# Kernel optimization log

Hardware: AMD Instinct MI355X
Metric: run time of the kernel (lower is better)

Reference implementation:

```python
import jax, jax.numpy as jnp
import numpy as np

N_KERNELS = 11

def _kernel_mus(n):
    l = [1.0]
    bs = 2.0 / (n - 1)
    l.append(1 - bs / 2)
    for i in range(1, n - 1):
        l.append(l[i] - bs)
    return l

def _kernel_sigmas(n):
    bs = 2.0 / (n - 1)
    return [0.001] + [0.5 * bs] * (n - 1)

MU = jnp.asarray(_kernel_mus(N_KERNELS), jnp.float32)      # [K]
SIGMA = jnp.asarray(_kernel_sigmas(N_KERNELS), jnp.float32)  # [K]


def setup_inputs() -> dict:
    key = jax.random.key(0)
    ks = jax.random.split(key, 10)
    V, E, C = 50000, 300, 128
    B, Q, D = 128, 30, 200
    inp = {
        'query_tokens': jax.random.randint(ks[0], (B, Q), 0, V),
        'document_tokens': jax.random.randint(ks[1], (B, D), 0, V),
        'embedding': jax.random.normal(ks[2], (V, E), jnp.float32) * 0.1,
        'conv_w1': jax.random.normal(ks[3], (C, E, 1), jnp.float32) * 0.05,
        'conv_w2': jax.random.normal(ks[4], (C, E, 2), jnp.float32) * 0.05,
        'conv_w3': jax.random.normal(ks[5], (C, E, 3), jnp.float32) * 0.05,
        'conv_b1': jax.random.normal(ks[6], (C,), jnp.float32) * 0.01,
        'conv_b2': jax.random.normal(ks[7], (C,), jnp.float32) * 0.01,
        'conv_b3': jax.random.normal(ks[8], (C,), jnp.float32) * 0.01,
        'dense_w': jax.random.uniform(ks[9], (1, N_KERNELS * 9), jnp.float32, -0.014, 0.014),
    }
    return inp


def _conv_ngram(x_ble, w, b):
    # x_ble: [B, L, E]; w: [C, E, k]; pad (0, k-1) on the length dim -> same length out
    x = x_ble.transpose(0, 2, 1)  # [B, E, L]
    y = jax.lax.conv_general_dilated(
        x, w, window_strides=(1,), padding=[(0, w.shape[2] - 1)],
        dimension_numbers=('NCH', 'OIH', 'NCH'))
    return jax.nn.relu(y + b[None, :, None]).transpose(0, 2, 1)  # [B, L, C]


def _kernel_pool(q, d, qd_mask, q_mask):
    # q: [B,Q,C], d: [B,D,C]; cosine sim -> Gaussian RBF soft-binning -> masked log-sum pooling
    qn = q / (jnp.linalg.norm(q, axis=-1, keepdims=True) + 1e-13)
    dn = d / (jnp.linalg.norm(d, axis=-1, keepdims=True) + 1e-13)
    cos = jnp.einsum('bqc,bdc->bqd', qn, dn) * qd_mask           # [B,Q,D]
    diff = cos[..., None] - MU                                    # [B,Q,D,K]
    kern = jnp.exp(-(diff * diff) / (2.0 * SIGMA * SIGMA)) * qd_mask[..., None]
    per_kernel_query = jnp.sum(kern, axis=2)                      # [B,Q,K]
    logk = jnp.log(jnp.clip(per_kernel_query, 1e-10)) * 0.01
    return jnp.sum(logk * q_mask[..., None], axis=1)              # [B,K]


def reference(query_tokens, document_tokens, embedding,
              conv_w1, conv_w2, conv_w3, conv_b1, conv_b2, conv_b3, dense_w):
    q_mask = (query_tokens > 0).astype(jnp.float32)               # [B,Q]
    d_mask = (document_tokens > 0).astype(jnp.float32)            # [B,D]
    qd_mask = q_mask[:, :, None] * d_mask[:, None, :]             # [B,Q,D]

    q_emb = embedding[query_tokens]                               # [B,Q,E]
    d_emb = embedding[document_tokens]                            # [B,D,E]

    convs = [(conv_w1, conv_b1), (conv_w2, conv_b2), (conv_w3, conv_b3)]
    q_grams = [_conv_ngram(q_emb, w, b) for w, b in convs]
    d_grams = [_conv_ngram(d_emb, w, b) for w, b in convs]

    feats = jnp.concatenate(
        [_kernel_pool(q, d, qd_mask, q_mask) for q in q_grams for d in d_grams],
        axis=1)                                                   # [B, K*9]
    return (feats @ dense_w.T)[:, 0]                              # [B]
```

## Files before the change

kernel.cpp:

```cpp
#include <hip/hip_runtime.h>
#include <hip/hip_bf16.h>
#include <math.h>

#define B_   128
#define Qn   30
#define Dn   200
#define En   300

typedef __attribute__((ext_vector_type(8))) short short8;
typedef __attribute__((ext_vector_type(4))) float floatx4;
typedef unsigned int u32;
typedef unsigned short u16;

static __device__ __forceinline__ u16 f2b(float x) {
    union { float f; u32 u; } v; v.f = x;
    u32 r = v.u + 0x7FFFu + ((v.u >> 16) & 1u);
    return (u16)(r >> 16);
}
static __device__ __forceinline__ float bits2f(u32 u) {
    union { u32 u2; float f; } v; v.u2 = u; return v.f;
}

__global__ void prep_kernel(
    const float* __restrict__ w1, const float* __restrict__ w2, const float* __restrict__ w3,
    u16* __restrict__ Wt3)
{
    int p = (blockIdx.x*128 + blockIdx.y)*256 + threadIdx.x;
    if (p >= 245760) return;
    int ks = p / 24576;
    int r  = p - ks*24576;
    int g, rr;
    if (r < 4096)        { g = 0; rr = r;         }
    else if (r < 12288)  { g = 1; rr = r - 4096;  }
    else                 { g = 2; rr = r - 12288; }
    int j  = rr >> 12;
    int r2 = rr & 4095;
    int nt  = r2 >> 9;
    int q4  = (r2 >> 7) & 3;
    int c16 = (r2 >> 3) & 15;
    int k8  = r2 & 7;
    int ch = nt*16 + c16;
    int e  = ks*32 + q4*8 + k8;
    float v = 0.f;
    if (e < En) {
        if (g == 0)      v = w1[ch*En + e];
        else if (g == 1) v = w2[(ch*En + e)*2 + j];
        else             v = w3[(ch*En + e)*3 + j];
    }
    Wt3[p] = f2b(v);
}

__global__ __launch_bounds__(512, 4) void conv_kernel(
    const int* __restrict__ qtok, const int* __restrict__ dtok,
    const float* __restrict__ emb,
    const u16* __restrict__ Wt3,
    const float* __restrict__ b1, const float* __restrict__ b2, const float* __restrict__ b3,
    u16* __restrict__ qg, u16* __restrict__ dg,
    float* __restrict__ invnq, float* __restrict__ invnd)
{
    __shared__ __align__(16) char smem[43560];
    char* As  = smem;
    int*  toks = (int*)(smem + 43296);

    const int tile = blockIdx.x;
    const int tid = threadIdx.x;
    const int wv = tid >> 6, lane = tid & 63;
    const int l15 = lane & 15, qd4 = lane >> 4;
    const int mh = wv >> 2, nh = wv & 3;
    const int gR0 = tile*64;

    if (tid < 66) {
        int gr = gR0 + tid;
        int t = -1;
        if (gr < 32768) {
            int b = gr >> 8, pos = gr & 255;
            if (pos < Dn) t = dtok[b*Dn + pos];
            else if (pos >= 208 && pos < 238) t = qtok[b*Qn + (pos - 208)];
        }
        toks[tid] = t;
    }
    __syncthreads();

    #pragma unroll
    for (int i = 0; i < 6; ++i) {
        int idx = tid + i*512;
        if (idx < 2640) {
            int r = idx / 40, c4 = idx - r*40;
            int t = toks[r];
            u16 o0=0,o1=0,o2=0,o3=0;
            if (t >= 0) {
                float4 v = *(const float4*)(emb + t*En + c4*4);
                o0=f2b(v.x); o1=f2b(v.y); o2=f2b(v.z); o3=f2b(v.w);
            }
            u16* pdst = (u16*)(As + r*656 + c4*8);
            pdst[0]=o0; pdst[1]=o1; pdst[2]=o2; pdst[3]=o3;
        }
    }

    float bias[3][2];
    #pragma unroll
    for (int nt = 0; nt < 2; ++nt) {
        int ch = nh*32 + nt*16 + l15;
        bias[0][nt] = b1[ch];
        bias[1][nt] = b2[ch];
        bias[2][nt] = b3[ch];
    }

    floatx4 acc[3][2][2];
    #pragma unroll
    for (int g = 0; g < 3; ++g)
        #pragma unroll
        for (int mt = 0; mt < 2; ++mt)
            #pragma unroll
            for (int nt = 0; nt < 2; ++nt)
                acc[g][mt][nt] = (floatx4){0.f,0.f,0.f,0.f};

    __syncthreads();

    float4 hf[6];
    #pragma unroll
    for (int i = 0; i < 6; ++i) {
        int idx = tid + i*512;
        const float* p = emb;
        if (idx < 2640) {
            int r = idx / 40, c = idx - r*40;
            int t = toks[r];
            if (t >= 0 && c < 35) p = emb + t*En + (40 + c)*4;
        }
        hf[i] = *(const float4*)p;
    }

    #pragma unroll 1
    for (int ks = 0; ks < 5; ++ks) {
        short8 af[2][3];
        #pragma unroll
        for (int mt = 0; mt < 2; ++mt)
            #pragma unroll
            for (int j = 0; j < 3; ++j)
                af[mt][j] = *(const short8*)(As + (mh*32 + mt*16 + l15 + j)*656 + ks*64 + qd4*16);
        const u16* Wks = Wt3 + ks*24576;
        #pragma unroll
        for (int g = 0; g < 3; ++g) {
            const int cbW = (g == 0) ? 0 : (g == 1) ? 4096 : 12288;
            #pragma unroll
            for (int j = 0; j <= g; ++j) {
                const u16* bb = Wks + cbW + (j*8 + nh*2)*512 + lane*8;
                short8 w0  = *(const short8*)(bb);
                short8 w1v = *(const short8*)(bb + 512);
                #pragma unroll
                for (int mt = 0; mt < 2; ++mt) {
                    acc[g][mt][0] = __builtin_amdgcn_mfma_f32_16x16x32_bf16(
                        af[mt][j], w0,  acc[g][mt][0], 0, 0, 0);
                    acc[g][mt][1] = __builtin_amdgcn_mfma_f32_16x16x32_bf16(
                        af[mt][j], w1v, acc[g][mt][1], 0, 0, 0);
                }
            }
        }
    }

    #pragma unroll
    for (int i = 0; i < 6; ++i) {
        int idx = tid + i*512;
        if (idx < 2640) {
            int r = idx / 40, c = idx - r*40;
            int t = toks[r];
            bool ok = (t >= 0) && (c < 35);
            u16 o0=0,o1=0,o2=0,o3=0;
            if (ok) { o0=f2b(hf[i].x); o1=f2b(hf[i].y); o2=f2b(hf[i].z); o3=f2b(hf[i].w); }
            u16* pdst = (u16*)(As + r*656 + (40 + c)*8);
            pdst[0]=o0; pdst[1]=o1; pdst[2]=o2; pdst[3]=o3;
        }
    }
    __syncthreads();

    #pragma unroll 1
    for (int ks = 5; ks < 10; ++ks) {
        short8 af[2][3];
        #pragma unroll
        for (int mt = 0; mt < 2; ++mt)
            #pragma unroll
            for (int j = 0; j < 3; ++j)
                af[mt][j] = *(const short8*)(As + (mh*32 + mt*16 + l15 + j)*656 + ks*64 + qd4*16);
        const u16* Wks = Wt3 + ks*24576;
        #pragma unroll
        for (int g = 0; g < 3; ++g) {
            const int cbW = (g == 0) ? 0 : (g == 1) ? 4096 : 12288;
            #pragma unroll
            for (int j = 0; j <= g; ++j) {
                const u16* bb = Wks + cbW + (j*8 + nh*2)*512 + lane*8;
                short8 w0  = *(const short8*)(bb);
                short8 w1v = *(const short8*)(bb + 512);
                #pragma unroll
                for (int mt = 0; mt < 2; ++mt) {
                    acc[g][mt][0] = __builtin_amdgcn_mfma_f32_16x16x32_bf16(
                        af[mt][j], w0,  acc[g][mt][0], 0, 0, 0);
                    acc[g][mt][1] = __builtin_amdgcn_mfma_f32_16x16x32_bf16(
                        af[mt][j], w1v, acc[g][mt][1], 0, 0, 0);
                }
            }
        }
    }

    u16* Gs = (u16*)smem;
    #pragma unroll
    for (int g = 0; g < 3; ++g) {
        __syncthreads();
        #pragma unroll
        for (int mt = 0; mt < 2; ++mt)
            #pragma unroll
            for (int nt = 0; nt < 2; ++nt) {
                int ch = nh*32 + nt*16 + l15;
                #pragma unroll
                for (int i = 0; i < 4; ++i) {
                    int row = mh*32 + mt*16 + qd4*4 + i;
                    Gs[row*136 + ch] = f2b(fmaxf(acc[g][mt][nt][i] + bias[g][nt], 0.f));
                }
            }
        __syncthreads();

        {
            int r = tid >> 3, pp = tid & 7;
            const char* rp = (const char*)Gs + r*272 + pp*32;
            float ssum = 0.f;
            #pragma unroll
            for (int t2 = 0; t2 < 2; ++t2) {
                uint4 u = *(const uint4*)(rp + t2*16);
                float x;
                x = bits2f(u.x << 16); ssum += x*x;  x = bits2f(u.x & 0xffff0000u); ssum += x*x;
                x = bits2f(u.y << 16); ssum += x*x;  x = bits2f(u.y & 0xffff0000u); ssum += x*x;
                x = bits2f(u.z << 16); ssum += x*x;  x = bits2f(u.z & 0xffff0000u); ssum += x*x;
                x = bits2f(u.w << 16); ssum += x*x;  x = bits2f(u.w & 0xffff0000u); ssum += x*x;
            }
            ssum += __shfl_xor(ssum, 1);
            ssum += __shfl_xor(ssum, 2);
            ssum += __shfl_xor(ssum, 4);
            if (pp == 0) {
                float inv = 1.f / (sqrtf(ssum) + 1e-13f);
                int gr = gR0 + r;
                int b = gr >> 8, pos = gr & 255;
                if (pos < 208)      invnd[(g*B_ + b)*208 + pos] = inv;
                else if (pos < 238) invnq[(g*B_ + b)*32 + (pos - 208)] = inv;
            }
        }
        #pragma unroll
        for (int i = 0; i < 2; ++i) {
            int idx = tid + i*512;
            int r = idx >> 4, c16 = idx & 15;
            uint4 v = *(const uint4*)((const char*)Gs + r*272 + c16*16);
            int gr = gR0 + r;
            int b = gr >> 8, pos = gr & 255;
            if (pos < 208)      *(uint4*)(dg + ((g*B_ + b)*208 + pos)*128 + c16*8) = v;
            else if (pos < 238) *(uint4*)(qg + ((g*B_ + b)*32 + (pos - 208))*128 + c16*8) = v;
        }
    }
}

__global__ __launch_bounds__(256, 4) void pool_kernel(
    const u16* __restrict__ qg, const u16* __restrict__ dg,
    const float* __restrict__ invnq, const float* __restrict__ invnd,
    const int* __restrict__ qtok, const int* __restrict__ dtok,
    float* __restrict__ feats)
{
    __shared__ float pk[32*12];
    __shared__ float invqA[32];
    __shared__ float qmA[32];
    __shared__ __align__(16) float invd[208];

    const int tid = threadIdx.x;
    const int b = blockIdx.y, dj = blockIdx.x, qi = blockIdx.z;
    const int wv = tid >> 6, lane = tid & 63;
    const int l15 = lane & 15, qd4 = lane >> 4;

    if (tid < 208) {
        float v = invnd[(dj*B_ + b)*208 + tid];
        bool ok = (tid < Dn) && (dtok[b*Dn + tid] > 0);
        invd[tid] = ok ? v : (-fabsf(v) - 1.0f);
    }
    if (tid < 32) {
        float v = invnq[(qi*B_ + b)*32 + tid];
        bool ok = (tid < Qn) && (qtok[b*Qn + tid] > 0);
        invqA[tid] = ok ? v : 0.f;
        qmA[tid] = ok ? 1.f : 0.f;
    }
    for (int i = tid; i < 32*12; i += 256) pk[i] = 0.f;
    __syncthreads();

    const float CkR[9] = {8886110.5f, 162754.79f, 2980.958f, 54.598150f, 1.0f,
                          0.018315639f, 3.3546263e-4f, 6.1442124e-6f, 1.1253517e-7f};

    {
        short8 qf[2][4];
        float vq[2];
        #pragma unroll
        for (int qt = 0; qt < 2; ++qt) {
            vq[qt] = invqA[qt*16 + l15];
            #pragma unroll
            for (int ks = 0; ks < 4; ++ks)
                qf[qt][ks] = *(const short8*)(qg + ((qi*B_ + b)*32 + qt*16 + l15)*128 + ks*32 + qd4*8);
        }
        float pkl[2][11];
        #pragma unroll
        for (int qt = 0; qt < 2; ++qt)
            #pragma unroll
            for (int k = 0; k < 11; ++k) pkl[qt][k] = 0.f;

        const u16* dbase = dg + (size_t)(dj*B_ + b)*208*128;
        for (int t = wv; t < 13; t += 4) {
            short8 af[4];
            #pragma unroll
            for (int ks = 0; ks < 4; ++ks)
                af[ks] = *(const short8*)(dbase + (t*16 + l15)*128 + ks*32 + qd4*8);
            floatx4 acc[2];
            acc[0] = (floatx4){0.f,0.f,0.f,0.f};
            acc[1] = (floatx4){0.f,0.f,0.f,0.f};
            #pragma unroll
            for (int ks = 0; ks < 4; ++ks)
                #pragma unroll
                for (int qt = 0; qt < 2; ++qt)
                    acc[qt] = __builtin_amdgcn_mfma_f32_16x16x32_bf16(af[ks], qf[qt][ks], acc[qt], 0, 0, 0);
            floatx4 iv4 = *(const floatx4*)(invd + t*16 + qd4*4);
            #pragma unroll
            for (int qt = 0; qt < 2; ++qt)
                #pragma unroll
                for (int i = 0; i < 4; ++i) {
                    float cs = acc[qt][i] * vq[qt] * iv4[i];
                    cs = (cs > 0.f) ? cs : 2.0f;
                    float t0 = cs - 1.0f;
                    float u  = cs - 0.9f;
                    float s0 = __expf(-500000.f * t0 * t0);
                    float e  = __expf(-50.f * u * u);
                    float rr = __expf(-20.f * cs);
                    pkl[qt][0] += s0;
                    pkl[qt][1] += e;
                    #pragma unroll
                    for (int kk = 0; kk < 9; ++kk) {
                        e = e * rr * CkR[kk];
                        pkl[qt][2 + kk] += e;
                    }
                }
        }
        #pragma unroll
        for (int qt = 0; qt < 2; ++qt)
            #pragma unroll
            for (int k = 0; k < 11; ++k) {
                float v = pkl[qt][k];
                v += __shfl_xor(v, 16);
                v += __shfl_xor(v, 32);
                if (qd4 == 0) atomicAdd(&pk[(qt*16 + l15)*12 + k], v);
            }
    }
    __syncthreads();

    if (tid < 11) {
        int k = tid;
        float s = 0.f;
        for (int q = 0; q < Qn; ++q)
            s += qmA[q] * 0.01f * __logf(fmaxf(pk[q*12 + k], 1e-10f));
        feats[(b*9 + qi*3 + dj)*11 + k] = s;
    }
}

__global__ void final_kernel(const float* __restrict__ feats,
                             const float* __restrict__ dw,
                             float* __restrict__ out) {
    int b = threadIdx.x;
    if (b < B_) {
        float s = 0.f;
        for (int f = 0; f < 99; ++f) s += feats[b*99 + f] * dw[f];
        out[b] = s;
    }
}

extern "C" void kernel_launch(void* const* d_in, const int* in_sizes, int n_in,
                              void* d_out, int out_size, void* d_ws, size_t ws_size,
                              hipStream_t stream) {
    const int*   qtok = (const int*)d_in[0];
    const int*   dtok = (const int*)d_in[1];
    const float* emb  = (const float*)d_in[2];
    const float* w1   = (const float*)d_in[3];
    const float* w2   = (const float*)d_in[4];
    const float* w3   = (const float*)d_in[5];
    const float* b1   = (const float*)d_in[6];
    const float* b2   = (const float*)d_in[7];
    const float* b3   = (const float*)d_in[8];
    const float* dw   = (const float*)d_in[9];
    float* out = (float*)d_out;

    char* w = (char*)d_ws;
    u16*   Wt3   = (u16*)w;
    u16*   qg    = (u16*)(w + 491520);
    u16*   dgm   = (u16*)(w + 3637248);
    float* invq_ = (float*)(w + 24084480);
    float* invd_ = (float*)(w + 24133632);
    float* feats = (float*)(w + 24453120);

    prep_kernel<<<dim3(8, B_), 256, 0, stream>>>(w1, w2, w3, Wt3);

    conv_kernel<<<dim3(512), 512, 0, stream>>>(
        qtok, dtok, emb, Wt3, b1, b2, b3, qg, dgm, invq_, invd_);

    pool_kernel<<<dim3(3, B_, 3), 256, 0, stream>>>(qg, dgm, invq_, invd_, qtok, dtok, feats);

    final_kernel<<<1, 128, 0, stream>>>(feats, dw, out);
}
```

Measured before the change: 161.6 us.

## Double-buffer conv weight fragments with explicit async loads and vmcnt waits

```diff
diff --git a/kernel.cpp b/kernel.cpp
--- a/kernel.cpp
+++ b/kernel.cpp
@@ -19,6 +19,12 @@
 }
 static __device__ __forceinline__ float bits2f(u32 u) {
     union { u32 u2; float f; } v; v.u2 = u; return v.f;
+}
+
+static __device__ __forceinline__ short8 gload16(const u16* p) {
+    short8 r;
+    asm volatile("global_load_dwordx4 %0, %1, off" : "=&v"(r) : "v"(p));
+    return r;
 }
 
 __global__ void prep_kernel(
@@ -50,7 +56,55 @@
     Wt3[p] = f2b(v);
 }
 
-__global__ __launch_bounds__(512, 4) void conv_kernel(
+#define MFMA __builtin_amdgcn_mfma_f32_16x16x32_bf16
+
+#define LOADB(P, KS) { \
+    const u16* _b = Wt3 + (KS)*24576 + nh*1024 + lane*8; \
+    P##0  = gload16(_b);          P##1  = gload16(_b + 512); \
+    P##2  = gload16(_b + 4096);   P##3  = gload16(_b + 4608); \
+    P##4  = gload16(_b + 8192);   P##5  = gload16(_b + 8704); \
+    P##6  = gload16(_b + 12288);  P##7  = gload16(_b + 12800); \
+    P##8  = gload16(_b + 16384);  P##9  = gload16(_b + 16896); \
+    P##10 = gload16(_b + 20480);  P##11 = gload16(_b + 20992); }
+
+#define AFLOAD(KS) \
+    short8 af00 = *(const short8*)(As + (mh*32 +  0 + l15 + 0)*656 + (KS)*64 + qd4*16); \
+    short8 af01 = *(const short8*)(As + (mh*32 +  0 + l15 + 1)*656 + (KS)*64 + qd4*16); \
+    short8 af02 = *(const short8*)(As + (mh*32 +  0 + l15 + 2)*656 + (KS)*64 + qd4*16); \
+    short8 af10 = *(const short8*)(As + (mh*32 + 16 + l15 + 0)*656 + (KS)*64 + qd4*16); \
+    short8 af11 = *(const short8*)(As + (mh*32 + 16 + l15 + 1)*656 + (KS)*64 + qd4*16); \
+    short8 af12 = *(const short8*)(As + (mh*32 + 16 + l15 + 2)*656 + (KS)*64 + qd4*16);
+
+#define VMWAIT12 { asm volatile("s_waitcnt vmcnt(12)" ::: "memory"); __builtin_amdgcn_sched_barrier(0); }
+#define VMWAIT0  { asm volatile("s_waitcnt vmcnt(0)"  ::: "memory"); __builtin_amdgcn_sched_barrier(0); }
+
+#define MFMAS(P) \
+    acc[0][0][0] = MFMA(af00, P##0,  acc[0][0][0], 0,0,0); \
+    acc[0][0][1] = MFMA(af00, P##1,  acc[0][0][1], 0,0,0); \
+    acc[0][1][0] = MFMA(af10, P##0,  acc[0][1][0], 0,0,0); \
+    acc[0][1][1] = MFMA(af10, P##1,  acc[0][1][1], 0,0,0); \
+    acc[1][0][0] = MFMA(af00, P##2,  acc[1][0][0], 0,0,0); \
+    acc[1][0][1] = MFMA(af00, P##3,  acc[1][0][1], 0,0,0); \
+    acc[1][1][0] = MFMA(af10, P##2,  acc[1][1][0], 0,0,0); \
+    acc[1][1][1] = MFMA(af10, P##3,  acc[1][1][1], 0,0,0); \
+    acc[1][0][0] = MFMA(af01, P##4,  acc[1][0][0], 0,0,0); \
+    acc[1][0][1] = MFMA(af01, P##5,  acc[1][0][1], 0,0,0); \
+    acc[1][1][0] = MFMA(af11, P##4,  acc[1][1][0], 0,0,0); \
+    acc[1][1][1] = MFMA(af11, P##5,  acc[1][1][1], 0,0,0); \
+    acc[2][0][0] = MFMA(af00, P##6,  acc[2][0][0], 0,0,0); \
+    acc[2][0][1] = MFMA(af00, P##7,  acc[2][0][1], 0,0,0); \
+    acc[2][1][0] = MFMA(af10, P##6,  acc[2][1][0], 0,0,0); \
+    acc[2][1][1] = MFMA(af10, P##7,  acc[2][1][1], 0,0,0); \
+    acc[2][0][0] = MFMA(af01, P##8,  acc[2][0][0], 0,0,0); \
+    acc[2][0][1] = MFMA(af01, P##9,  acc[2][0][1], 0,0,0); \
+    acc[2][1][0] = MFMA(af11, P##8,  acc[2][1][0], 0,0,0); \
+    acc[2][1][1] = MFMA(af11, P##9,  acc[2][1][1], 0,0,0); \
+    acc[2][0][0] = MFMA(af02, P##10, acc[2][0][0], 0,0,0); \
+    acc[2][0][1] = MFMA(af02, P##11, acc[2][0][1], 0,0,0); \
+    acc[2][1][0] = MFMA(af12, P##10, acc[2][1][0], 0,0,0); \
+    acc[2][1][1] = MFMA(af12, P##11, acc[2][1][1], 0,0,0);
+
+__global__ __launch_bounds__(512, 2) void conv_kernel(
     const int* __restrict__ qtok, const int* __restrict__ dtok,
     const float* __restrict__ emb,
     const u16* __restrict__ Wt3,
@@ -130,33 +184,15 @@
         hf[i] = *(const float4*)p;
     }
 
-    #pragma unroll 1
-    for (int ks = 0; ks < 5; ++ks) {
-        short8 af[2][3];
-        #pragma unroll
-        for (int mt = 0; mt < 2; ++mt)
-            #pragma unroll
-            for (int j = 0; j < 3; ++j)
-                af[mt][j] = *(const short8*)(As + (mh*32 + mt*16 + l15 + j)*656 + ks*64 + qd4*16);
-        const u16* Wks = Wt3 + ks*24576;
-        #pragma unroll
-        for (int g = 0; g < 3; ++g) {
-            const int cbW = (g == 0) ? 0 : (g == 1) ? 4096 : 12288;
-            #pragma unroll
-            for (int j = 0; j <= g; ++j) {
-                const u16* bb = Wks + cbW + (j*8 + nh*2)*512 + lane*8;
-                short8 w0  = *(const short8*)(bb);
-                short8 w1v = *(const short8*)(bb + 512);
-                #pragma unroll
-                for (int mt = 0; mt < 2; ++mt) {
-                    acc[g][mt][0] = __builtin_amdgcn_mfma_f32_16x16x32_bf16(
-                        af[mt][j], w0,  acc[g][mt][0], 0, 0, 0);
-                    acc[g][mt][1] = __builtin_amdgcn_mfma_f32_16x16x32_bf16(
-                        af[mt][j], w1v, acc[g][mt][1], 0, 0, 0);
-                }
-            }
-        }
-    }
+    short8 wa0,wa1,wa2,wa3,wa4,wa5,wa6,wa7,wa8,wa9,wa10,wa11;
+    short8 wb0,wb1,wb2,wb3,wb4,wb5,wb6,wb7,wb8,wb9,wb10,wb11;
+
+    LOADB(wa, 0)
+    { LOADB(wb, 1) AFLOAD(0) VMWAIT12 MFMAS(wa) }
+    { LOADB(wa, 2) AFLOAD(1) VMWAIT12 MFMAS(wb) }
+    { LOADB(wb, 3) AFLOAD(2) VMWAIT12 MFMAS(wa) }
+    { LOADB(wa, 4) AFLOAD(3) VMWAIT12 MFMAS(wb) }
+    { LOADB(wb, 5) AFLOAD(4) VMWAIT12 MFMAS(wa) }
 
     #pragma unroll
     for (int i = 0; i < 6; ++i) {
@@ -173,33 +209,11 @@
     }
     __syncthreads();
 
-    #pragma unroll 1
-    for (int ks = 5; ks < 10; ++ks) {
-        short8 af[2][3];
-        #pragma unroll
-        for (int mt = 0; mt < 2; ++mt)
-            #pragma unroll
-            for (int j = 0; j < 3; ++j)
-                af[mt][j] = *(const short8*)(As + (mh*32 + mt*16 + l15 + j)*656 + ks*64 + qd4*16);
-        const u16* Wks = Wt3 + ks*24576;
-        #pragma unroll
-        for (int g = 0; g < 3; ++g) {
-            const int cbW = (g == 0) ? 0 : (g == 1) ? 4096 : 12288;
-            #pragma unroll
-            for (int j = 0; j <= g; ++j) {
-                const u16* bb = Wks + cbW + (j*8 + nh*2)*512 + lane*8;
-                short8 w0  = *(const short8*)(bb);
-                short8 w1v = *(const short8*)(bb + 512);
-                #pragma unroll
-                for (int mt = 0; mt < 2; ++mt) {
-                    acc[g][mt][0] = __builtin_amdgcn_mfma_f32_16x16x32_bf16(
-                        af[mt][j], w0,  acc[g][mt][0], 0, 0, 0);
-                    acc[g][mt][1] = __builtin_amdgcn_mfma_f32_16x16x32_bf16(
-                        af[mt][j], w1v, acc[g][mt][1], 0, 0, 0);
-                }
-            }
-        }
-    }
+    { LOADB(wa, 6) AFLOAD(5) VMWAIT12 MFMAS(wb) }
+    { LOADB(wb, 7) AFLOAD(6) VMWAIT12 MFMAS(wa) }
+    { LOADB(wa, 8) AFLOAD(7) VMWAIT12 MFMAS(wb) }
+    { LOADB(wb, 9) AFLOAD(8) VMWAIT12 MFMAS(wa) }
+    {              AFLOAD(9) VMWAIT0  MFMAS(wb) }
 
     u16* Gs = (u16*)smem;
     #pragma unroll
```

Measured after the change: 170.7 us. +5.7%, slower.

## Prefetch all pool-kernel tiles upfront with inline asm loads and staged waitcnts

Applied to the files above, without the earlier changes.

```diff
diff --git a/kernel.cpp b/kernel.cpp
--- a/kernel.cpp
+++ b/kernel.cpp
@@ -20,6 +20,14 @@
 static __device__ __forceinline__ float bits2f(u32 u) {
     union { u32 u2; float f; } v; v.u2 = u; return v.f;
 }
+
+static __device__ __forceinline__ short8 gload16(const u16* p) {
+    short8 r;
+    asm volatile("global_load_dwordx4 %0, %1, off" : "=&v"(r) : "v"(p));
+    return r;
+}
+
+#define MFMA __builtin_amdgcn_mfma_f32_16x16x32_bf16
 
 __global__ void prep_kernel(
     const float* __restrict__ w1, const float* __restrict__ w2, const float* __restrict__ w3,
@@ -149,10 +157,8 @@
                 short8 w1v = *(const short8*)(bb + 512);
                 #pragma unroll
                 for (int mt = 0; mt < 2; ++mt) {
-                    acc[g][mt][0] = __builtin_amdgcn_mfma_f32_16x16x32_bf16(
-                        af[mt][j], w0,  acc[g][mt][0], 0, 0, 0);
-                    acc[g][mt][1] = __builtin_amdgcn_mfma_f32_16x16x32_bf16(
-                        af[mt][j], w1v, acc[g][mt][1], 0, 0, 0);
+                    acc[g][mt][0] = MFMA(af[mt][j], w0,  acc[g][mt][0], 0, 0, 0);
+                    acc[g][mt][1] = MFMA(af[mt][j], w1v, acc[g][mt][1], 0, 0, 0);
                 }
             }
         }
@@ -192,10 +198,8 @@
                 short8 w1v = *(const short8*)(bb + 512);
                 #pragma unroll
                 for (int mt = 0; mt < 2; ++mt) {
-                    acc[g][mt][0] = __builtin_amdgcn_mfma_f32_16x16x32_bf16(
-                        af[mt][j], w0,  acc[g][mt][0], 0, 0, 0);
-                    acc[g][mt][1] = __builtin_amdgcn_mfma_f32_16x16x32_bf16(
-                        af[mt][j], w1v, acc[g][mt][1], 0, 0, 0);
+                    acc[g][mt][0] = MFMA(af[mt][j], w0,  acc[g][mt][0], 0, 0, 0);
+                    acc[g][mt][1] = MFMA(af[mt][j], w1v, acc[g][mt][1], 0, 0, 0);
                 }
             }
         }
@@ -255,7 +259,7 @@
     }
 }
 
-__global__ __launch_bounds__(256, 4) void pool_kernel(
+__global__ __launch_bounds__(256, 2) void pool_kernel(
     const u16* __restrict__ qg, const u16* __restrict__ dg,
     const float* __restrict__ invnq, const float* __restrict__ invnd,
     const int* __restrict__ qtok, const int* __restrict__ dtok,
@@ -288,67 +292,100 @@
     const float CkR[9] = {8886110.5f, 162754.79f, 2980.958f, 54.598150f, 1.0f,
                           0.018315639f, 3.3546263e-4f, 6.1442124e-6f, 1.1253517e-7f};
 
-    {
-        short8 qf[2][4];
-        float vq[2];
-        #pragma unroll
-        for (int qt = 0; qt < 2; ++qt) {
-            vq[qt] = invqA[qt*16 + l15];
-            #pragma unroll
-            for (int ks = 0; ks < 4; ++ks)
-                qf[qt][ks] = *(const short8*)(qg + ((qi*B_ + b)*32 + qt*16 + l15)*128 + ks*32 + qd4*8);
-        }
-        float pkl[2][11];
-        #pragma unroll
-        for (int qt = 0; qt < 2; ++qt)
-            #pragma unroll
-            for (int k = 0; k < 11; ++k) pkl[qt][k] = 0.f;
-
-        const u16* dbase = dg + (size_t)(dj*B_ + b)*208*128;
-        for (int t = wv; t < 13; t += 4) {
-            short8 af[4];
-            #pragma unroll
-            for (int ks = 0; ks < 4; ++ks)
-                af[ks] = *(const short8*)(dbase + (t*16 + l15)*128 + ks*32 + qd4*8);
-            floatx4 acc[2];
-            acc[0] = (floatx4){0.f,0.f,0.f,0.f};
-            acc[1] = (floatx4){0.f,0.f,0.f,0.f};
-            #pragma unroll
-            for (int ks = 0; ks < 4; ++ks)
-                #pragma unroll
-                for (int qt = 0; qt < 2; ++qt)
-                    acc[qt] = __builtin_amdgcn_mfma_f32_16x16x32_bf16(af[ks], qf[qt][ks], acc[qt], 0, 0, 0);
-            floatx4 iv4 = *(const floatx4*)(invd + t*16 + qd4*4);
-            #pragma unroll
-            for (int qt = 0; qt < 2; ++qt)
-                #pragma unroll
-                for (int i = 0; i < 4; ++i) {
-                    float cs = acc[qt][i] * vq[qt] * iv4[i];
-                    cs = (cs > 0.f) ? cs : 2.0f;
-                    float t0 = cs - 1.0f;
-                    float u  = cs - 0.9f;
-                    float s0 = __expf(-500000.f * t0 * t0);
-                    float e  = __expf(-50.f * u * u);
-                    float rr = __expf(-20.f * cs);
-                    pkl[qt][0] += s0;
-                    pkl[qt][1] += e;
-                    #pragma unroll
-                    for (int kk = 0; kk < 9; ++kk) {
-                        e = e * rr * CkR[kk];
-                        pkl[qt][2 + kk] += e;
-                    }
-                }
-        }
-        #pragma unroll
-        for (int qt = 0; qt < 2; ++qt)
-            #pragma unroll
-            for (int k = 0; k < 11; ++k) {
-                float v = pkl[qt][k];
-                v += __shfl_xor(v, 16);
-                v += __shfl_xor(v, 32);
-                if (qd4 == 0) atomicAdd(&pk[(qt*16 + l15)*12 + k], v);
-            }
-    }
+    const u16* qbase = qg + (size_t)((qi*B_ + b)*32)*128 + l15*128 + qd4*8;
+    const u16* dbase = dg + (size_t)(dj*B_ + b)*208*128 + l15*128 + qd4*8;
+    const int t0 = wv, t1 = wv + 4, t2 = wv + 8;
+    const int t3 = (wv == 0) ? 12 : 11;
+
+    short8 q00 = gload16(qbase + 0*32);
+    short8 q01 = gload16(qbase + 1*32);
+    short8 q02 = gload16(qbase + 2*32);
+    short8 q03 = gload16(qbase + 3*32);
+    short8 q10 = gload16(qbase + 16*128 + 0*32);
+    short8 q11 = gload16(qbase + 16*128 + 1*32);
+    short8 q12 = gload16(qbase + 16*128 + 2*32);
+    short8 q13 = gload16(qbase + 16*128 + 3*32);
+    short8 a00 = gload16(dbase + t0*2048 + 0*32);
+    short8 a01 = gload16(dbase + t0*2048 + 1*32);
+    short8 a02 = gload16(dbase + t0*2048 + 2*32);
+    short8 a03 = gload16(dbase + t0*2048 + 3*32);
+    short8 a10 = gload16(dbase + t1*2048 + 0*32);
+    short8 a11 = gload16(dbase + t1*2048 + 1*32);
+    short8 a12 = gload16(dbase + t1*2048 + 2*32);
+    short8 a13 = gload16(dbase + t1*2048 + 3*32);
+    short8 a20 = gload16(dbase + t2*2048 + 0*32);
+    short8 a21 = gload16(dbase + t2*2048 + 1*32);
+    short8 a22 = gload16(dbase + t2*2048 + 2*32);
+    short8 a23 = gload16(dbase + t2*2048 + 3*32);
+    short8 a30 = gload16(dbase + t3*2048 + 0*32);
+    short8 a31 = gload16(dbase + t3*2048 + 1*32);
+    short8 a32 = gload16(dbase + t3*2048 + 2*32);
+    short8 a33 = gload16(dbase + t3*2048 + 3*32);
+
+    float vq0 = invqA[l15], vq1 = invqA[16 + l15];
+
+    float pkl[2][11];
+    #pragma unroll
+    for (int qt = 0; qt < 2; ++qt)
+        #pragma unroll
+        for (int k = 0; k < 11; ++k) pkl[qt][k] = 0.f;
+
+    #define PITER(A0, A1, A2, A3, TT, VMSTR)                                  \
+    {                                                                         \
+        asm volatile("s_waitcnt vmcnt(" VMSTR ")" ::: "memory");              \
+        __builtin_amdgcn_sched_barrier(0);                                    \
+        floatx4 ac0 = (floatx4){0.f,0.f,0.f,0.f};                             \
+        floatx4 ac1 = (floatx4){0.f,0.f,0.f,0.f};                             \
+        ac0 = MFMA(A0, q00, ac0, 0,0,0); ac1 = MFMA(A0, q10, ac1, 0,0,0);     \
+        ac0 = MFMA(A1, q01, ac0, 0,0,0); ac1 = MFMA(A1, q11, ac1, 0,0,0);     \
+        ac0 = MFMA(A2, q02, ac0, 0,0,0); ac1 = MFMA(A2, q12, ac1, 0,0,0);     \
+        ac0 = MFMA(A3, q03, ac0, 0,0,0); ac1 = MFMA(A3, q13, ac1, 0,0,0);     \
+        floatx4 iv4 = *(const floatx4*)(invd + (TT)*16 + qd4*4);              \
+        _Pragma("unroll")                                                     \
+        for (int i = 0; i < 4; ++i) {                                         \
+            float cs = ac0[i] * vq0 * iv4[i];                                 \
+            cs = (cs > 0.f) ? cs : 2.0f;                                      \
+            float tt0 = cs - 1.0f, uu = cs - 0.9f;                            \
+            float s0 = __expf(-500000.f * tt0 * tt0);                         \
+            float e  = __expf(-50.f * uu * uu);                               \
+            float rr = __expf(-20.f * cs);                                    \
+            pkl[0][0] += s0; pkl[0][1] += e;                                  \
+            _Pragma("unroll")                                                 \
+            for (int kk = 0; kk < 9; ++kk) {                                  \
+                e = e * rr * CkR[kk]; pkl[0][2 + kk] += e;                    \
+            }                                                                 \
+        }                                                                     \
+        _Pragma("unroll")                                                     \
+        for (int i = 0; i < 4; ++i) {                                         \
+            float cs = ac1[i] * vq1 * iv4[i];                                 \
+            cs = (cs > 0.f) ? cs : 2.0f;                                      \
+            float tt0 = cs - 1.0f, uu = cs - 0.9f;                            \
+            float s0 = __expf(-500000.f * tt0 * tt0);                         \
+            float e  = __expf(-50.f * uu * uu);                               \
+            float rr = __expf(-20.f * cs);                                    \
+            pkl[1][0] += s0; pkl[1][1] += e;                                  \
+            _Pragma("unroll")                                                 \
+            for (int kk = 0; kk < 9; ++kk) {                                  \
+                e = e * rr * CkR[kk]; pkl[1][2 + kk] += e;                    \
+            }                                                                 \
+        }                                                                     \
+    }
+
+    PITER(a00, a01, a02, a03, t0, "12")
+    PITER(a10, a11, a12, a13, t1, "8")
+    PITER(a20, a21, a22, a23, t2, "4")
+    if (wv == 0) { PITER(a30, a31, a32, a33, t3, "0") }
+    #undef PITER
+
+    #pragma unroll
+    for (int qt = 0; qt < 2; ++qt)
+        #pragma unroll
+        for (int k = 0; k < 11; ++k) {
+            float v = pkl[qt][k];
+            v += __shfl_xor(v, 16);
+            v += __shfl_xor(v, 32);
+            if (qd4 == 0) atomicAdd(&pk[(qt*16 + l15)*12 + k], v);
+        }
     __syncthreads();
 
     if (tid < 11) {
```

Result: no change. 160.6 us (-0.6%).
